# Kernel tuning notes

Hardware: AMD Instinct MI355X
Metric: run time of the kernel (lower is better)

Reference implementation:

```python
import jax, jax.numpy as jnp
import numpy as np
from jax.scipy.linalg import expm

B, T, D = 4096, 256, 64


def setup_inputs() -> dict:
    key = jax.random.key(0)
    k1, k2, k3 = jax.random.split(key, 3)
    inputs = jax.random.normal(k1, (B, T, D), dtype=jnp.float32)
    time = jax.random.uniform(k2, (T,), dtype=jnp.float32)  # TIME grid in [0,1)
    kernel = jax.random.normal(k3, (D, D), dtype=jnp.float32) * 0.1  # learned Koopman generator
    return {"inputs": inputs, "time": time, "kernel": kernel}


def reference(inputs, time, kernel):
    # expm(kernel * t) for every t, batched instead of a Python loop: [T, D, D]
    mats = jax.vmap(lambda t: expm(kernel * t))(time)
    # original: einsum('ijk,lk->lij', mats, inputs[:, 0, :]) -> [B, T, D]
    x0 = inputs[:, 0, :]  # [B, D] initial condition
    trajs = jnp.einsum('tij,bj->bti', mats, x0)
    return trajs
```

## Files before the change

### kernel.cpp

```cpp
#include <hip/hip_runtime.h>
#include <math.h>


#define TT 256
#define DD 64
#define BB 4096
#define S1 68
#define LD 72
#define THETA 0.5f
#define MTERMS 10

typedef __attribute__((ext_vector_type(8))) short short8;
typedef __attribute__((ext_vector_type(4))) float f32x4;


__device__ __forceinline__ void mm68(const float* __restrict__ Lt,
                                     const float* __restrict__ R,
                                     float* __restrict__ C,
                                     float f, float* __restrict__ Eacc, int tid) {
    const int i0 = (tid & 15) * 4;
    const int j0 = (tid >> 4) * 4;
    float acc[4][4];
#pragma unroll
    for (int r = 0; r < 4; ++r)
#pragma unroll
        for (int c = 0; c < 4; ++c) acc[r][c] = 0.f;

#pragma unroll 8
    for (int k = 0; k < 64; ++k) {
        const float4 a = *reinterpret_cast<const float4*>(&Lt[k * S1 + i0]);
        const float4 b = *reinterpret_cast<const float4*>(&R[k * S1 + j0]);
        const float av[4] = {a.x, a.y, a.z, a.w};
        const float bv[4] = {b.x, b.y, b.z, b.w};
#pragma unroll
        for (int r = 0; r < 4; ++r)
#pragma unroll
            for (int c = 0; c < 4; ++c) acc[r][c] = fmaf(av[r], bv[c], acc[r][c]);
    }

#pragma unroll
    for (int r = 0; r < 4; ++r) {
        float4 v;
        v.x = acc[r][0] * f; v.y = acc[r][1] * f; v.z = acc[r][2] * f; v.w = acc[r][3] * f;
        *reinterpret_cast<float4*>(&C[(i0 + r) * S1 + j0]) = v;
        if (Eacc) {
            float* e = &Eacc[(i0 + r) * S1 + j0];
            e[0] += v.x; e[1] += v.y; e[2] += v.z; e[3] += v.w;
        }
    }
}

__device__ __forceinline__ void transpose68(const float* __restrict__ X,
                                            float* __restrict__ XT, int tid) {
    const int i = tid >> 2;
    const int j0 = (tid & 3) * 16;
#pragma unroll
    for (int c4 = 0; c4 < 4; ++c4) {
        const float4 v = *reinterpret_cast<const float4*>(&X[i * S1 + j0 + 4 * c4]);
        XT[(j0 + 4 * c4 + 0) * S1 + i] = v.x;
        XT[(j0 + 4 * c4 + 1) * S1 + i] = v.y;
        XT[(j0 + 4 * c4 + 2) * S1 + i] = v.z;
        XT[(j0 + 4 * c4 + 3) * S1 + i] = v.w;
    }
}

__global__ __launch_bounds__(256)
void expm_kernel(const float* __restrict__ K, const float* __restrict__ tim,
                 float* __restrict__ G) {
    __shared__ float As[64 * S1];
    __shared__ float Pa[64 * S1];
    __shared__ float Pb[64 * S1];
    __shared__ float Et[64 * S1];
    __shared__ float Tx[64 * S1];
    __shared__ float red[64];

    const int tid = threadIdx.x;
    const int t = blockIdx.x;
    const float tval = tim[t];

    if (tid < 64) {
        float s = 0.f;
        for (int j = 0; j < 64; ++j) s += fabsf(K[tid * 64 + j]);
        red[tid] = s;
    }
    __syncthreads();
    if (tid == 0) {
        float m = 0.f;
        for (int i = 0; i < 64; ++i) m = fmaxf(m, red[i]);
        const float nt = m * tval;
        int s = 0;
        if (nt > THETA) {
            s = (int)ceilf(log2f(nt / THETA));
            if (s < 0) s = 0;
        }
        red[0] = ldexpf(tval, -s);
        red[1] = (float)s;
    }
    __syncthreads();
    const float scale = red[0];
    const int sq = (int)red[1];
    __syncthreads();

    {
        const int i = tid >> 2;
        const int j0 = (tid & 3) * 16;
#pragma unroll
        for (int c = 0; c < 16; ++c) {
            const int j = j0 + c;
            const float v = K[i * 64 + j] * scale;
            As[i * S1 + j] = v;
            Pa[j * S1 + i] = v;
            Et[j * S1 + i] = v + ((i == j) ? 1.f : 0.f);
        }
    }
    __syncthreads();

    float* Pcur = Pa;
    float* Pnext = Pb;
    for (int n = 2; n <= MTERMS; ++n) {
        mm68(As, Pcur, Pnext, 1.0f / (float)n, Et, tid);
        __syncthreads();
        float* tmp = Pcur; Pcur = Pnext; Pnext = tmp;
    }

    transpose68(Et, Tx, tid);
    __syncthreads();
    float* cur = Tx;
    float* nxt = Pa;
    const float* curT = Et;
    for (int r = 0; r < sq; ++r) {
        if (r > 0) {
            transpose68(cur, Pb, tid);
            __syncthreads();
            curT = Pb;
        }
        mm68(curT, cur, nxt, 1.f, nullptr, tid);
        __syncthreads();
        float* tmp = cur; cur = nxt; nxt = tmp;
    }

    {
        const int i = tid >> 2;
        const int j0 = (tid & 3) * 16;
        float* outp = G + (size_t)t * 4096 + i * 64 + j0;
#pragma unroll
        for (int c4 = 0; c4 < 4; ++c4) {
            *reinterpret_cast<float4*>(outp + 4 * c4) =
                *reinterpret_cast<const float4*>(&cur[i * S1 + j0 + 4 * c4]);
        }
    }
}


__device__ __forceinline__ void bf16_split(float x, unsigned short& hi, unsigned short& lo) {
    union { float f; unsigned int u; } a; a.f = x;
    unsigned int r = (a.u + 0x7fffu + ((a.u >> 16) & 1u)) & 0xffff0000u;
    hi = (unsigned short)(r >> 16);
    union { float f; unsigned int u; } d; d.f = x - __uint_as_float(r);
    lo = (unsigned short)(d.u >> 16);
}

__global__ __launch_bounds__(256)
void traj_mfma(const float* __restrict__ inputs, const float* __restrict__ G,
               float* __restrict__ out) {
    __shared__ unsigned short Ahi[64 * LD];
    __shared__ unsigned short Alo[64 * LD];
    __shared__ unsigned short Bhi[64 * LD];
    __shared__ unsigned short Blo[64 * LD];

    const int tid = threadIdx.x;
    const int t  = blockIdx.x & (TT - 1);
    const int b0 = (blockIdx.x >> 8) * 64;

    {
        const int row  = tid >> 2;
        const int col0 = (tid & 3) * 16;
        const float* asrc = inputs + (size_t)(b0 + row) * (TT * DD) + col0;
        const float* bsrc = G + (size_t)t * 4096 + row * 64 + col0;
#pragma unroll
        for (int c = 0; c < 4; ++c) {
            const float4 va = *reinterpret_cast<const float4*>(asrc + 4 * c);
            const float4 vb = *reinterpret_cast<const float4*>(bsrc + 4 * c);
            ushort4 ah, al, bh, bl;
            bf16_split(va.x, ah.x, al.x); bf16_split(va.y, ah.y, al.y);
            bf16_split(va.z, ah.z, al.z); bf16_split(va.w, ah.w, al.w);
            bf16_split(vb.x, bh.x, bl.x); bf16_split(vb.y, bh.y, bl.y);
            bf16_split(vb.z, bh.z, bl.z); bf16_split(vb.w, bh.w, bl.w);
            const int o = row * LD + col0 + 4 * c;
            *reinterpret_cast<ushort4*>(&Ahi[o]) = ah;
            *reinterpret_cast<ushort4*>(&Alo[o]) = al;
            *reinterpret_cast<ushort4*>(&Bhi[o]) = bh;
            *reinterpret_cast<ushort4*>(&Blo[o]) = bl;
        }
    }
    __syncthreads();

    const int w  = tid >> 6;
    const int ln = tid & 15;
    const int qd = (tid >> 4) & 3;

    f32x4 acc[4];
#pragma unroll
    for (int nt = 0; nt < 4; ++nt) acc[nt] = (f32x4){0.f, 0.f, 0.f, 0.f};

#pragma unroll
    for (int kh = 0; kh < 2; ++kh) {
        const int ko = kh * 32 + qd * 8;
        const short8 ah = *reinterpret_cast<const short8*>(&Ahi[(w * 16 + ln) * LD + ko]);
        const short8 al = *reinterpret_cast<const short8*>(&Alo[(w * 16 + ln) * LD + ko]);
#pragma unroll
        for (int nt = 0; nt < 4; ++nt) {
            const short8 bh = *reinterpret_cast<const short8*>(&Bhi[(nt * 16 + ln) * LD + ko]);
            const short8 bl = *reinterpret_cast<const short8*>(&Blo[(nt * 16 + ln) * LD + ko]);
            acc[nt] = __builtin_amdgcn_mfma_f32_16x16x32_bf16(ah, bh, acc[nt], 0, 0, 0);
            acc[nt] = __builtin_amdgcn_mfma_f32_16x16x32_bf16(ah, bl, acc[nt], 0, 0, 0);
            acc[nt] = __builtin_amdgcn_mfma_f32_16x16x32_bf16(al, bh, acc[nt], 0, 0, 0);
        }
    }

    float* obase = out + (size_t)(b0 + w * 16 + qd * 4) * (TT * DD) + (size_t)t * DD + ln;
#pragma unroll
    for (int r = 0; r < 4; ++r) {
#pragma unroll
        for (int nt = 0; nt < 4; ++nt) {
            obase[(size_t)r * (TT * DD) + nt * 16] = acc[nt][r];
        }
    }
}

extern "C" void kernel_launch(void* const* d_in, const int* in_sizes, int n_in,
                              void* d_out, int out_size, void* d_ws, size_t ws_size,
                              hipStream_t stream) {
    const float* inputs = (const float*)d_in[0];
    const float* tim    = (const float*)d_in[1];
    const float* K      = (const float*)d_in[2];
    float* out = (float*)d_out;
    float* G   = (float*)d_ws;

    expm_kernel<<<TT, 256, 0, stream>>>(K, tim, G);
    traj_mfma<<<(BB / 64) * TT, 256, 0, stream>>>(inputs, G, out);
}
```

Measured before the change: 442.4 us.

## Precompute bf16 hi/lo splits in expm kernel and load MFMA fragments directly

The expm kernel now also converts the initial condition x0 and each exponential matrix into bf16 hi/lo pairs and writes them to workspace. The trajectory kernel drops its shared-memory staging and per-block conversion, loads MFMA fragments straight from global memory, and keeps the matrix fragments in registers while each wave handles 64 batch rows. The MFMA operands are swapped so each lane writes contiguous float4 outputs. This removes the conversions repeated across blocks and the scattered scalar stores, at the cost of more register pressure and uncoalesced short8 fragment loads from global memory.

```diff
diff --git a/kernel.cpp b/kernel.cpp
--- a/kernel.cpp
+++ b/kernel.cpp
@@ -6,12 +6,19 @@
 #define DD 64
 #define BB 4096
 #define S1 68
-#define LD 72
 #define THETA 0.5f
 #define MTERMS 10
 
 typedef __attribute__((ext_vector_type(8))) short short8;
 typedef __attribute__((ext_vector_type(4))) float f32x4;
+
+__device__ __forceinline__ void bf16_split(float x, unsigned short& hi, unsigned short& lo) {
+    union { float f; unsigned int u; } a; a.f = x;
+    unsigned int r = (a.u + 0x7fffu + ((a.u >> 16) & 1u)) & 0xffff0000u;
+    hi = (unsigned short)(r >> 16);
+    union { float f; unsigned int u; } d; d.f = x - __uint_as_float(r);
+    lo = (unsigned short)(d.u >> 16);
+}
 
 
 __device__ __forceinline__ void mm68(const float* __restrict__ Lt,
@@ -66,7 +73,9 @@
 
 __global__ __launch_bounds__(256)
 void expm_kernel(const float* __restrict__ K, const float* __restrict__ tim,
-                 float* __restrict__ G) {
+                 const float* __restrict__ inputs,
+                 unsigned short* __restrict__ Bh, unsigned short* __restrict__ Bl,
+                 unsigned short* __restrict__ Ah, unsigned short* __restrict__ Al) {
     __shared__ float As[64 * S1];
     __shared__ float Pa[64 * S1];
     __shared__ float Pb[64 * S1];
@@ -77,6 +86,18 @@
     const int tid = threadIdx.x;
     const int t = blockIdx.x;
     const float tval = tim[t];
+
+    {
+        const int idx = t * 1024 + tid * 4;
+        const int b = idx >> 6;
+        const int j = idx & 63;
+        const float4 v = *reinterpret_cast<const float4*>(inputs + (size_t)b * (TT * DD) + j);
+        ushort4 h, l;
+        bf16_split(v.x, h.x, l.x); bf16_split(v.y, h.y, l.y);
+        bf16_split(v.z, h.z, l.z); bf16_split(v.w, h.w, l.w);
+        *reinterpret_cast<ushort4*>(&Ah[b * 64 + j]) = h;
+        *reinterpret_cast<ushort4*>(&Al[b * 64 + j]) = l;
+    }
 
     if (tid < 64) {
         float s = 0.f;
@@ -142,88 +163,77 @@
     {
         const int i = tid >> 2;
         const int j0 = (tid & 3) * 16;
-        float* outp = G + (size_t)t * 4096 + i * 64 + j0;
+        unsigned short* oh = Bh + (size_t)t * 4096 + i * 64 + j0;
+        unsigned short* ol = Bl + (size_t)t * 4096 + i * 64 + j0;
 #pragma unroll
         for (int c4 = 0; c4 < 4; ++c4) {
-            *reinterpret_cast<float4*>(outp + 4 * c4) =
-                *reinterpret_cast<const float4*>(&cur[i * S1 + j0 + 4 * c4]);
-        }
-    }
-}
-
-
-__device__ __forceinline__ void bf16_split(float x, unsigned short& hi, unsigned short& lo) {
-    union { float f; unsigned int u; } a; a.f = x;
-    unsigned int r = (a.u + 0x7fffu + ((a.u >> 16) & 1u)) & 0xffff0000u;
-    hi = (unsigned short)(r >> 16);
-    union { float f; unsigned int u; } d; d.f = x - __uint_as_float(r);
-    lo = (unsigned short)(d.u >> 16);
-}
+            const float4 v = *reinterpret_cast<const float4*>(&cur[i * S1 + j0 + 4 * c4]);
+            ushort4 h, l;
+            bf16_split(v.x, h.x, l.x); bf16_split(v.y, h.y, l.y);
+            bf16_split(v.z, h.z, l.z); bf16_split(v.w, h.w, l.w);
+            *reinterpret_cast<ushort4*>(oh + 4 * c4) = h;
+            *reinterpret_cast<ushort4*>(ol + 4 * c4) = l;
+        }
+    }
+}
+
 
 __global__ __launch_bounds__(256)
-void traj_mfma(const float* __restrict__ inputs, const float* __restrict__ G,
+void traj_mfma(const unsigned short* __restrict__ Ah, const unsigned short* __restrict__ Al,
+               const unsigned short* __restrict__ Bh, const unsigned short* __restrict__ Bl,
                float* __restrict__ out) {
-    __shared__ unsigned short Ahi[64 * LD];
-    __shared__ unsigned short Alo[64 * LD];
-    __shared__ unsigned short Bhi[64 * LD];
-    __shared__ unsigned short Blo[64 * LD];
-
     const int tid = threadIdx.x;
     const int t  = blockIdx.x & (TT - 1);
-    const int b0 = (blockIdx.x >> 8) * 64;
-
-    {
-        const int row  = tid >> 2;
-        const int col0 = (tid & 3) * 16;
-        const float* asrc = inputs + (size_t)(b0 + row) * (TT * DD) + col0;
-        const float* bsrc = G + (size_t)t * 4096 + row * 64 + col0;
-#pragma unroll
-        for (int c = 0; c < 4; ++c) {
-            const float4 va = *reinterpret_cast<const float4*>(asrc + 4 * c);
-            const float4 vb = *reinterpret_cast<const float4*>(bsrc + 4 * c);
-            ushort4 ah, al, bh, bl;
-            bf16_split(va.x, ah.x, al.x); bf16_split(va.y, ah.y, al.y);
-            bf16_split(va.z, ah.z, al.z); bf16_split(va.w, ah.w, al.w);
-            bf16_split(vb.x, bh.x, bl.x); bf16_split(vb.y, bh.y, bl.y);
-            bf16_split(vb.z, bh.z, bl.z); bf16_split(vb.w, bh.w, bl.w);
-            const int o = row * LD + col0 + 4 * c;
-            *reinterpret_cast<ushort4*>(&Ahi[o]) = ah;
-            *reinterpret_cast<ushort4*>(&Alo[o]) = al;
-            *reinterpret_cast<ushort4*>(&Bhi[o]) = bh;
-            *reinterpret_cast<ushort4*>(&Blo[o]) = bl;
-        }
-    }
-    __syncthreads();
-
+    const int bg = blockIdx.x >> 8;
     const int w  = tid >> 6;
-    const int ln = tid & 15;
-    const int qd = (tid >> 4) & 3;
-
-    f32x4 acc[4];
-#pragma unroll
-    for (int nt = 0; nt < 4; ++nt) acc[nt] = (f32x4){0.f, 0.f, 0.f, 0.f};
-
-#pragma unroll
-    for (int kh = 0; kh < 2; ++kh) {
-        const int ko = kh * 32 + qd * 8;
-        const short8 ah = *reinterpret_cast<const short8*>(&Ahi[(w * 16 + ln) * LD + ko]);
-        const short8 al = *reinterpret_cast<const short8*>(&Alo[(w * 16 + ln) * LD + ko]);
-#pragma unroll
-        for (int nt = 0; nt < 4; ++nt) {
-            const short8 bh = *reinterpret_cast<const short8*>(&Bhi[(nt * 16 + ln) * LD + ko]);
-            const short8 bl = *reinterpret_cast<const short8*>(&Blo[(nt * 16 + ln) * LD + ko]);
-            acc[nt] = __builtin_amdgcn_mfma_f32_16x16x32_bf16(ah, bh, acc[nt], 0, 0, 0);
-            acc[nt] = __builtin_amdgcn_mfma_f32_16x16x32_bf16(ah, bl, acc[nt], 0, 0, 0);
-            acc[nt] = __builtin_amdgcn_mfma_f32_16x16x32_bf16(al, bh, acc[nt], 0, 0, 0);
-        }
-    }
-
-    float* obase = out + (size_t)(b0 + w * 16 + qd * 4) * (TT * DD) + (size_t)t * DD + ln;
-#pragma unroll
-    for (int r = 0; r < 4; ++r) {
-#pragma unroll
-        for (int nt = 0; nt < 4; ++nt) {
-            obase[(size_t)r * (TT * DD) + nt * 16] = acc[nt][r];
+    const int l  = tid & 63;
+    const int ln = l & 15;
+    const int qd = l >> 4;
+
+    const unsigned short* mh = Bh + (size_t)t * 4096;
+    const unsigned short* ml = Bl + (size_t)t * 4096;
+    short8 Mh[4][2], Ml[4][2];
+#pragma unroll
+    for (int m = 0; m < 4; ++m)
+#pragma unroll
+        for (int kh = 0; kh < 2; ++kh) {
+            const int off = (m * 16 + ln) * 64 + kh * 32 + qd * 8;
+            Mh[m][kh] = *reinterpret_cast<const short8*>(mh + off);
+            Ml[m][kh] = *reinterpret_cast<const short8*>(ml + off);
+        }
+
+    const int brow0 = bg * 256 + w * 64;
+#pragma unroll
+    for (int it = 0; it < 4; ++it) {
+        const int brow = brow0 + it * 16 + ln;
+
+        short8 Xh[2], Xl[2];
+#pragma unroll
+        for (int kh = 0; kh < 2; ++kh) {
+            const int aoff = brow * 64 + kh * 32 + qd * 8;
+            Xh[kh] = *reinterpret_cast<const short8*>(Ah + aoff);
+            Xl[kh] = *reinterpret_cast<const short8*>(Al + aoff);
+        }
+
+        f32x4 acc[4];
+#pragma unroll
+        for (int m = 0; m < 4; ++m) acc[m] = (f32x4){0.f, 0.f, 0.f, 0.f};
+
+#pragma unroll
+        for (int kh = 0; kh < 2; ++kh)
+#pragma unroll
+            for (int m = 0; m < 4; ++m) {
+                acc[m] = __builtin_amdgcn_mfma_f32_16x16x32_bf16(Mh[m][kh], Xh[kh], acc[m], 0, 0, 0);
+                acc[m] = __builtin_amdgcn_mfma_f32_16x16x32_bf16(Ml[m][kh], Xh[kh], acc[m], 0, 0, 0);
+                acc[m] = __builtin_amdgcn_mfma_f32_16x16x32_bf16(Mh[m][kh], Xl[kh], acc[m], 0, 0, 0);
+            }
+
+        float* obase = out + (size_t)brow * (TT * DD) + (size_t)t * DD + qd * 4;
+#pragma unroll
+        for (int m = 0; m < 4; ++m) {
+            float4 v;
+            v.x = acc[m][0]; v.y = acc[m][1]; v.z = acc[m][2]; v.w = acc[m][3];
+            *reinterpret_cast<float4*>(obase + m * 16) = v;
         }
     }
 }
@@ -235,8 +245,12 @@
     const float* tim    = (const float*)d_in[1];
     const float* K      = (const float*)d_in[2];
     float* out = (float*)d_out;
-    float* G   = (float*)d_ws;
-
-    expm_kernel<<<TT, 256, 0, stream>>>(K, tim, G);
-    traj_mfma<<<(BB / 64) * TT, 256, 0, stream>>>(inputs, G, out);
-}
+
+    unsigned short* Bh = (unsigned short*)d_ws;
+    unsigned short* Bl = Bh + (size_t)TT * DD * DD;
+    unsigned short* Ah = Bl + (size_t)TT * DD * DD;
+    unsigned short* Al = Ah + (size_t)BB * DD;
+
+    expm_kernel<<<TT, 256, 0, stream>>>(K, tim, inputs, Bh, Bl, Ah, Al);
+    traj_mfma<<<(BB / 256) * TT, 256, 0, stream>>>(Ah, Al, Bh, Bl, out);
+}
```

Measured after the change: 447.7 us. No clear change (+1.2%).
